# Kernel tuning notes

Measured on AMD Instinct MI355X. Metric: run time of the kernel, lower is better.

Reference implementation:

```python
import jax, jax.numpy as jnp
import numpy as np

_GELU = lambda x: jax.nn.gelu(x, approximate=False)  # torch nn.GELU default = exact erf


def setup_inputs():
    key = jax.random.key(0)
    ks = jax.random.split(key, 32)
    B, H = 16384, 768
    def p(i, shape):
        return jax.random.normal(ks[i], shape, jnp.float32) * 0.02
    return {
        "image_feat": jax.random.normal(ks[0], (B, H), jnp.float32),
        "text_feat": jax.random.normal(ks[1], (B, H), jnp.float32),
        "enhanced_image_feat": jax.random.normal(ks[2], (B, H), jnp.float32),
        "enhanced_text_feat": jax.random.normal(ks[3], (B, H), jnp.float32),
        "missing_type": jax.random.randint(ks[4], (B,), 0, 4),
        # info_encoder: H->256->64
        "info_w1": p(5, (H, 256)), "info_b1": jnp.zeros((256,), jnp.float32),
        "info_w2": p(6, (256, 64)), "info_b2": jnp.zeros((64,), jnp.float32),
        # modality_importance_predictor: H->H/2->1 (dropout inactive at eval)
        "imp_w1": p(7, (H, H // 2)), "imp_b1": jnp.zeros((H // 2,), jnp.float32),
        "imp_w2": p(8, (H // 2, 1)), "imp_b2": jnp.zeros((1,), jnp.float32),
        # feature_discriminator: H->256->64->1
        "disc_w1": p(9, (H, 256)), "disc_b1": jnp.zeros((256,), jnp.float32),
        "disc_w2": p(10, (256, 64)), "disc_b2": jnp.zeros((64,), jnp.float32),
        "disc_w3": p(11, (64, 1)), "disc_b3": jnp.zeros((1,), jnp.float32),
        # consistency_predictor: 2H->H->H/2->1
        "cons_w1": p(12, (2 * H, H)), "cons_b1": jnp.zeros((H,), jnp.float32),
        "cons_w2": p(13, (H, H // 2)), "cons_b2": jnp.zeros((H // 2,), jnp.float32),
        "cons_w3": p(14, (H // 2, 1)), "cons_b3": jnp.zeros((1,), jnp.float32),
        # task_difficulty_predictor: 2H->H->H/2->1
        "diff_w1": p(15, (2 * H, H)), "diff_b1": jnp.zeros((H,), jnp.float32),
        "diff_w2": p(16, (H, H // 2)), "diff_b2": jnp.zeros((H // 2,), jnp.float32),
        "diff_w3": p(17, (H // 2, 1)), "diff_b3": jnp.zeros((1,), jnp.float32),
    }


def _forward(image_feat, text_feat, enhanced_image_feat, enhanced_text_feat,
             info_w1, info_b1, info_w2, info_b2,
             imp_w1, imp_b1, imp_w2, imp_b2,
             disc_w1, disc_b1, disc_w2, disc_b2, disc_w3, disc_b3,
             cons_w1, cons_b1, cons_w2, cons_b2, cons_w3, cons_b3,
             diff_w1, diff_b1, diff_w2, diff_b2, diff_w3, diff_b3):
    sig = jax.nn.sigmoid

    def geometric(f):  # vectorized version of the per-sample python loop
        n = jnp.linalg.norm(f, axis=-1)
        nq = sig((n - 1.0) * 2.0)
        sp = jnp.mean((jnp.abs(f) > 0.01).astype(jnp.float32), axis=-1)
        sq = sig(jnp.std(f, axis=-1, ddof=1) * 10.0 - 1.0)  # torch.std is unbiased
        return (nq + sp + sq) / 3.0

    def information(f):
        enc = _GELU(f @ info_w1 + info_b1) @ info_w2 + info_b2  # [B,64]
        disc = jnp.round(sig(enc) * 10.0).astype(jnp.int32)     # values in 0..10
        # histogram-based entropy == the torch.unique loop (prob = count/64)
        counts = jnp.sum(disc[:, :, None] == jnp.arange(11, dtype=jnp.int32)[None, None, :], axis=1)
        prob = counts.astype(jnp.float32) / enc.shape[-1]
        ent = -jnp.sum(jnp.where(prob > 0, prob * jnp.log(prob + 1e-8), 0.0), axis=-1)
        eq = sig(ent - 2.0)
        # svd of a 1xD matrix has a single singular value = ||f||_2
        n = jnp.linalg.norm(f, axis=-1)
        cq = (n > 0.01).astype(jnp.float32) / f.shape[-1]
        fn = f / jnp.maximum(n, 1e-12)[:, None]  # F.normalize
        dq = sig(jnp.sum(fn * fn, axis=-1) - 0.5)
        return (eq + cq + dq) / 3.0

    def importance(f):
        return sig(_GELU(f @ imp_w1 + imp_b1) @ imp_w2 + imp_b2)[:, 0]

    def discrim(f):
        h = _GELU(f @ disc_w1 + disc_b1)
        h = _GELU(h @ disc_w2 + disc_b2)
        return sig(h @ disc_w3 + disc_b3)[:, 0]

    def head3(f, w1, b1, w2, b2, w3, b3):
        h = _GELU(f @ w1 + b1)
        h = _GELU(h @ w2 + b2)
        return sig(h @ w3 + b3)[:, 0]

    g_img = geometric(image_feat)
    g_txt = geometric(text_feat)
    g_eimg = geometric(enhanced_image_feat)
    g_etxt = geometric(enhanced_text_feat)
    i_img = information(image_feat)
    i_txt = information(text_feat)
    cons_o = head3(jnp.concatenate([image_feat, text_feat], -1), cons_w1, cons_b1, cons_w2, cons_b2, cons_w3, cons_b3)
    cons_e = head3(jnp.concatenate([enhanced_image_feat, enhanced_text_feat], -1), cons_w1, cons_b1, cons_w2, cons_b2, cons_w3, cons_b3)
    imp_i = importance(image_feat)
    imp_t = importance(text_feat)
    imp_ei = importance(enhanced_image_feat)
    imp_et = importance(enhanced_text_feat)
    auth_io = discrim(image_feat)
    auth_ie = discrim(enhanced_image_feat)
    auth_to = discrim(text_feat)
    auth_te = discrim(enhanced_text_feat)
    diff = head3(jnp.concatenate([enhanced_image_feat, enhanced_text_feat], -1), diff_w1, diff_b1, diff_w2, diff_b2, diff_w3, diff_b3)
    overall = (g_img + g_txt + i_img + i_txt + cons_e + (imp_i + imp_t) / 2.0) / 6.0
    return jnp.stack([g_img, g_txt, g_eimg, g_etxt, i_img, i_txt, cons_o, cons_e,
                      imp_i, imp_t, imp_ei, imp_et, auth_io, auth_ie, auth_to, auth_te,
                      diff, overall])  # [18, B]


def reference(image_feat, text_feat, enhanced_image_feat, enhanced_text_feat, missing_type,
              info_w1, info_b1, info_w2, info_b2,
              imp_w1, imp_b1, imp_w2, imp_b2,
              disc_w1, disc_b1, disc_w2, disc_b2, disc_w3, disc_b3,
              cons_w1, cons_b1, cons_w2, cons_b2, cons_w3, cons_b3,
              diff_w1, diff_b1, diff_w2, diff_b2, diff_w3, diff_b3):
    # missing_type is carried by the original forward but never used in the math
    return _forward(image_feat, text_feat, enhanced_image_feat, enhanced_text_feat,
                    info_w1, info_b1, info_w2, info_b2,
                    imp_w1, imp_b1, imp_w2, imp_b2,
                    disc_w1, disc_b1, disc_w2, disc_b2, disc_w3, disc_b3,
                    cons_w1, cons_b1, cons_w2, cons_b2, cons_w3, cons_b3,
                    diff_w1, diff_b1, diff_w2, diff_b2, diff_w3, diff_b3)
```

## Files before the change

kernel.cpp:

```cpp
#include <hip/hip_runtime.h>

typedef unsigned short bfu;
typedef __attribute__((ext_vector_type(8))) __bf16 bf16x8;
typedef __attribute__((ext_vector_type(4))) float f32x4;

__device__ __forceinline__ float bf2f(bfu u) {
    unsigned int x = ((unsigned int)u) << 16;
    return __builtin_bit_cast(float, x);
}
__device__ __forceinline__ bfu f2bf(float f) {
    unsigned int u = __builtin_bit_cast(unsigned int, f);
    unsigned int r = (u + 0x7fffu + ((u >> 16) & 1u)) >> 16;
    return (bfu)r;
}
__device__ __forceinline__ float sigm(float x) { return 1.0f / (1.0f + __expf(-x)); }
__device__ __forceinline__ float gelu_f(float x) {
    const float y = 0.7978845608f * (x + 0.044715f * x * x * x);
    const float t = 1.f - 2.f / (__expf(2.f * y) + 1.f);
    return 0.5f * x * (1.f + t);
}
__device__ __forceinline__ float gelu_x(float x) {
    return 0.5f * x * (1.0f + erff(x * 0.70710678118654752f));
}

__device__ __forceinline__ void async16(const void* g, void* l) {
    __builtin_amdgcn_global_load_lds((const __attribute__((address_space(1))) void*)g,
                                     (__attribute__((address_space(3))) void*)l, 16, 0, 0);
}

struct TDesc { const float* src; bfu* dst; int K, N, blk0; };
struct TPack { TDesc d[9]; };

__global__ __launch_bounds__(256) void transpose_k(TPack p) {
    const int bid = blockIdx.x;
    int j = 0;
#pragma unroll
    for (int i = 1; i < 9; ++i)
        if (bid >= p.d[i].blk0) j = i;
    const TDesc d = p.d[j];
    const int local = bid - d.blk0;
    const int tkn = d.K >> 6;
    const int tk = local % tkn, tn = local / tkn;
    const int k0 = tk * 64, n0 = tn * 64;
    __shared__ float tile[64][65];
    const int tx = threadIdx.x & 63, ty = threadIdx.x >> 6;
#pragma unroll
    for (int i = 0; i < 16; ++i) {
        const int r = ty * 16 + i;
        tile[r][tx] = d.src[(size_t)(k0 + r) * d.N + n0 + tx];
    }
    __syncthreads();
#pragma unroll
    for (int i = 0; i < 16; ++i) {
        const int n = ty * 16 + i;
        d.dst[(size_t)(n0 + n) * d.K + k0 + tx] = f2bf(tile[tx][n]);
    }
}

__global__ __launch_bounds__(256)
void prep_k(float* accz, int nacc, bfu* disc2pad, const float* w3,
            const float* b2, float* w3pad, float* b2pad) {
    const int i = blockIdx.x * 256 + threadIdx.x;
    if (i < nacc) accz[i] = 0.f;
    if (i < 64 * 256) disc2pad[64 * 256 + i] = 0;
    if (i < 128) {
        w3pad[i] = (i < 64) ? w3[i] : 0.f;
        b2pad[i] = (i < 64) ? b2[i] : 0.f;
    }
}

__global__ __launch_bounds__(256)
void geomcast_k(const float* F0, const float* F1, bfu* D0, bfu* D1,
                float* g0, float* g1, float* p0, float* p1) {
    const int z = blockIdx.y;
    const float* F = z ? F1 : F0;
    bfu* D = z ? D1 : D0;
    float* gout = z ? g1 : g0;
    float* part = z ? p1 : p0;
    const int wave = threadIdx.x >> 6, lane = threadIdx.x & 63;
    const int row = blockIdx.x * 4 + wave;
    const float* fr = F + (size_t)row * 768;
    bfu* dr = D + (size_t)row * 768;
    float sum = 0.f, ss = 0.f, cnt = 0.f;
#pragma unroll
    for (int i = 0; i < 3; ++i) {
        const float4 v = *(const float4*)(fr + i * 256 + lane * 4);
        sum += v.x + v.y + v.z + v.w;
        ss += v.x * v.x + v.y * v.y + v.z * v.z + v.w * v.w;
        cnt += ((fabsf(v.x) > 0.01f) ? 1.f : 0.f) + ((fabsf(v.y) > 0.01f) ? 1.f : 0.f) +
               ((fabsf(v.z) > 0.01f) ? 1.f : 0.f) + ((fabsf(v.w) > 0.01f) ? 1.f : 0.f);
        ushort4 b;
        b.x = f2bf(v.x); b.y = f2bf(v.y); b.z = f2bf(v.z); b.w = f2bf(v.w);
        *(ushort4*)(dr + i * 256 + lane * 4) = b;
    }
#pragma unroll
    for (int off = 32; off; off >>= 1) {
        sum += __shfl_xor(sum, off);
        ss  += __shfl_xor(ss, off);
        cnt += __shfl_xor(cnt, off);
    }
    if (lane == 0) {
        const float n = sqrtf(ss);
        const float nq = sigm((n - 1.f) * 2.f);
        const float sp = cnt * (1.f / 768.f);
        float var = (ss - sum * sum * (1.f / 768.f)) * (1.f / 767.f);
        var = fmaxf(var, 0.f);
        const float sq = sigm(sqrtf(var) * 10.f - 1.f);
        gout[row] = (nq + sp + sq) * (1.f / 3.f);
        if (part) {
            const float cq = (n > 0.01f) ? (1.f / 768.f) : 0.f;
            const float nc = fmaxf(n, 1e-12f);
            const float dq = sigm(ss / (nc * nc) - 0.5f);
            part[row] = (cq + dq) * (1.f / 3.f);
        }
    }
}

struct Seg {
    const bfu* A; const bfu* A2;
    const bfu* W;
    const float* bias;
    const float* dotw;
    bfu* C;
    float* acc;
    int ldc, mode, K, Ksplit, lda, Mtiles;
};
struct SegPack { Seg s[13]; };

__global__ __launch_bounds__(256)
void gemm_k(SegPack p) {
    constexpr int BK = 64, MT = 4, NT = 4;
    __shared__ bfu As[128 * BK];
    __shared__ bfu Ws[128 * BK];
    const int NTt = gridDim.x;
    const int g = blockIdx.y * NTt + blockIdx.x;
    const int G8 = NTt * 8;
    const int m = (g / G8) * 8 + (g & 7);
    const int n = (g % G8) >> 3;
    const Seg sg = p.s[n];
    if (m >= sg.Mtiles) return;
    const int t = threadIdx.x;
    const int wave = t >> 6, lane = t & 63;
    const int row_l = lane & 15, kq = lane >> 4;
    const int m0 = m * 128;
    const int wm = wave >> 1, wn = wave & 1;
    const int wrow0 = wm * 64, wcol0 = wn * 64;

    const int r0 = t >> 3;
    const int cc = ((t & 7) ^ (r0 & 7)) << 3;
    const size_t strA = (size_t)32 * sg.lda;
    const size_t strW = (size_t)32 * sg.K;
    const bfu* pA[4];
    const bfu* pW[4];
#pragma unroll
    for (int i = 0; i < 4; ++i) {
        pA[i] = sg.A + (size_t)(m0 + r0) * sg.lda + cc + i * strA;
        pW[i] = sg.W + (size_t)r0 * sg.K + cc + i * strW;
    }
    const int nkt = sg.K >> 6;
    const int ktsw = (sg.Ksplit < sg.K) ? (sg.Ksplit >> 6) : 0x7fffffff;

    f32x4 acc[MT][NT] = {};

    for (int kt = 0; kt < nkt; ++kt) {
        if (kt == ktsw) {
#pragma unroll
            for (int i = 0; i < 4; ++i)
                pA[i] = sg.A2 + (size_t)(m0 + r0) * sg.lda + cc + i * strA;
        }
#pragma unroll
        for (int i = 0; i < 4; ++i)
            async16(pA[i], As + ((i * 256 + wave * 64) << 3));
#pragma unroll
        for (int i = 0; i < 4; ++i)
            async16(pW[i], Ws + ((i * 256 + wave * 64) << 3));
        __syncthreads();
#pragma unroll
        for (int ks = 0; ks < 2; ++ks) {
            bf16x8 af[MT], bfr[NT];
#pragma unroll
            for (int mi = 0; mi < MT; ++mi) {
                const int rA = wrow0 + mi * 16 + row_l;
                af[mi] = *(const bf16x8*)(As + rA * BK + (((ks * 4 + kq) ^ (rA & 7)) << 3));
            }
#pragma unroll
            for (int ni = 0; ni < NT; ++ni) {
                const int rB = wcol0 + ni * 16 + row_l;
                bfr[ni] = *(const bf16x8*)(Ws + rB * BK + (((ks * 4 + kq) ^ (rB & 7)) << 3));
            }
#pragma unroll
            for (int mi = 0; mi < MT; ++mi)
#pragma unroll
                for (int ni = 0; ni < NT; ++ni)
                    acc[mi][ni] = __builtin_amdgcn_mfma_f32_16x16x32_bf16(af[mi], bfr[ni], acc[mi][ni], 0, 0, 0);
        }
        __syncthreads();
#pragma unroll
        for (int i = 0; i < 4; ++i) { pA[i] += BK; pW[i] += BK; }
    }

    if (sg.mode == 0) {
#pragma unroll
        for (int ni = 0; ni < NT; ++ni) {
            const int col = wcol0 + ni * 16 + row_l;
            const float bv = sg.bias[col];
#pragma unroll
            for (int mi = 0; mi < MT; ++mi)
#pragma unroll
                for (int r = 0; r < 4; ++r) {
                    const int row = m0 + wrow0 + mi * 16 + kq * 4 + r;
                    sg.C[(size_t)row * sg.ldc + col] = f2bf(gelu_f(acc[mi][ni][r] + bv));
                }
        }
    } else if (sg.mode == 2) {
#pragma unroll
        for (int ni = 0; ni < NT; ++ni) {
            const int col = wcol0 + ni * 16 + row_l;
            const float bv = sg.bias[col];
#pragma unroll
            for (int mi = 0; mi < MT; ++mi)
#pragma unroll
                for (int r = 0; r < 4; ++r) {
                    const int row = m0 + wrow0 + mi * 16 + kq * 4 + r;
                    sg.C[(size_t)row * sg.ldc + col] = f2bf(gelu_x(acc[mi][ni][r] + bv));
                }
        }
    } else {
#pragma unroll
        for (int mi = 0; mi < MT; ++mi)
#pragma unroll
            for (int r = 0; r < 4; ++r) {
                float s = 0.f;
#pragma unroll
                for (int ni = 0; ni < NT; ++ni) {
                    const int col = wcol0 + ni * 16 + row_l;
                    s += sg.dotw[col] * gelu_f(acc[mi][ni][r] + sg.bias[col]);
                }
                s += __shfl_xor(s, 1); s += __shfl_xor(s, 2);
                s += __shfl_xor(s, 4); s += __shfl_xor(s, 8);
                if (row_l == 0)
                    atomicAdd(sg.acc + m0 + wrow0 + mi * 16 + kq * 4 + r, s);
            }
    }
}

__global__ __launch_bounds__(256)
void gemm64ent_k(const bfu* __restrict__ A, const bfu* __restrict__ W,
                 const float* __restrict__ bias, const float* __restrict__ part,
                 float* out, int B, int K, int lda) {
    constexpr int BK = 64, MT = 2, NT = 4;
    __shared__ __align__(16) float smemf[8320];
    bfu* As = (bfu*)smemf;
    bfu* Ws = (bfu*)smemf + 128 * BK;
    float* ET = smemf;
    const int t = threadIdx.x;
    const int wave = t >> 6, lane = t & 63;
    const int row_l = lane & 15, kq = lane >> 4;
    const int m0 = blockIdx.x * 128;
    const int wrow0 = wave * 32;
    f32x4 acc[MT][NT] = {};
    const int nkt = K / BK;
    for (int kt = 0; kt < nkt; ++kt) {
        const int k0 = kt * BK;
#pragma unroll
        for (int i = 0; i < 4; ++i) {
            const int c = i * 256 + t;
            const int r = c >> 3, s = c & 7;
            const int cc = (s ^ (r & 7)) << 3;
            async16(A + (size_t)(m0 + r) * lda + k0 + cc, As + ((i * 256 + wave * 64) << 3));
        }
#pragma unroll
        for (int i = 0; i < 2; ++i) {
            const int c = i * 256 + t;
            const int r = c >> 3, s = c & 7;
            const int cc = (s ^ (r & 7)) << 3;
            async16(W + (size_t)r * K + k0 + cc, Ws + ((i * 256 + wave * 64) << 3));
        }
        __syncthreads();
#pragma unroll
        for (int ks = 0; ks < 2; ++ks) {
            bf16x8 af[MT], bfr[NT];
#pragma unroll
            for (int mi = 0; mi < MT; ++mi) {
                const int rA = wrow0 + mi * 16 + row_l;
                af[mi] = *(const bf16x8*)(As + rA * BK + (((ks * 4 + kq) ^ (rA & 7)) << 3));
            }
#pragma unroll
            for (int ni = 0; ni < NT; ++ni) {
                const int rB = ni * 16 + row_l;
                bfr[ni] = *(const bf16x8*)(Ws + rB * BK + (((ks * 4 + kq) ^ (rB & 7)) << 3));
            }
#pragma unroll
            for (int mi = 0; mi < MT; ++mi)
#pragma unroll
                for (int ni = 0; ni < NT; ++ni)
                    acc[mi][ni] = __builtin_amdgcn_mfma_f32_16x16x32_bf16(af[mi], bfr[ni], acc[mi][ni], 0, 0, 0);
        }
        __syncthreads();
    }
#pragma unroll
    for (int mi = 0; mi < MT; ++mi)
#pragma unroll
        for (int ni = 0; ni < NT; ++ni) {
            const int col = ni * 16 + row_l;
            const float bv = bias[col];
#pragma unroll
            for (int r = 0; r < 4; ++r)
                ET[(wrow0 + mi * 16 + kq * 4 + r) * 65 + col] = acc[mi][ni][r] + bv;
        }
    __syncthreads();
    if (t < 128) {
        int cnt[11];
#pragma unroll
        for (int b = 0; b < 11; ++b) cnt[b] = 0;
        for (int j = 0; j < 64; ++j) {
            const int d = (int)rintf(sigm(ET[t * 65 + j]) * 10.f);
#pragma unroll
            for (int b = 0; b < 11; ++b) cnt[b] += (d == b);
        }
        float ent = 0.f;
#pragma unroll
        for (int b = 0; b < 11; ++b) {
            if (cnt[b] > 0) {
                const float pp = (float)cnt[b] * (1.f / 64.f);
                ent -= pp * __logf(pp + 1e-8f);
            }
        }
        const int row = m0 + t;
        const int orow = (row < B) ? 4 : 5;
        const int rl = (row < B) ? row : row - B;
        out[(size_t)orow * B + rl] = part[row] + sigm(ent - 2.f) * (1.f / 3.f);
    }
}

__global__ __launch_bounds__(256)
void finalize_k(float* out, const float* a_imp1, const float* a_imp2,
                const float* a_co, const float* a_ce, const float* a_df,
                const float* a_d1, const float* a_d2,
                const float* imp_b2, const float* disc_b3,
                const float* cons_b3, const float* diff_b3, int B) {
    const int i = blockIdx.x * 256 + threadIdx.x;
    if (i >= B) return;
    const float ib = imp_b2[0], db = disc_b3[0], cb = cons_b3[0], fb = diff_b3[0];
    const float o6 = sigm(a_co[i] + cb);
    const float o7 = sigm(a_ce[i] + cb);
    const float o8 = sigm(a_imp1[i] + ib);
    const float o9 = sigm(a_imp1[B + i] + ib);
    out[6 * B + i] = o6;
    out[7 * B + i] = o7;
    out[8 * B + i] = o8;
    out[9 * B + i] = o9;
    out[10 * B + i] = sigm(a_imp2[i] + ib);
    out[11 * B + i] = sigm(a_imp2[B + i] + ib);
    out[12 * B + i] = sigm(a_d1[i] + db);
    out[14 * B + i] = sigm(a_d1[B + i] + db);
    out[13 * B + i] = sigm(a_d2[i] + db);
    out[15 * B + i] = sigm(a_d2[B + i] + db);
    out[16 * B + i] = sigm(a_df[i] + fb);
    const float v = out[0 * B + i] + out[1 * B + i] + out[4 * B + i] + out[5 * B + i] +
                    o7 + 0.5f * (o8 + o9);
    out[17 * B + i] = v * (1.f / 6.f);
}

extern "C" void kernel_launch(void* const* d_in, const int* in_sizes, int n_in,
                              void* d_out, int out_size, void* d_ws, size_t ws_size,
                              hipStream_t stream) {
    const int B = in_sizes[4];
    const int B2 = 2 * B;
    float* out = (float*)d_out;
    const float* img  = (const float*)d_in[0];
    const float* txt  = (const float*)d_in[1];
    const float* eimg = (const float*)d_in[2];
    const float* etxt = (const float*)d_in[3];
    const float* info_w1 = (const float*)d_in[5];  const float* info_b1 = (const float*)d_in[6];
    const float* info_w2 = (const float*)d_in[7];  const float* info_b2 = (const float*)d_in[8];
    const float* imp_w1  = (const float*)d_in[9];  const float* imp_b1  = (const float*)d_in[10];
    const float* imp_w2  = (const float*)d_in[11]; const float* imp_b2  = (const float*)d_in[12];
    const float* disc_w1 = (const float*)d_in[13]; const float* disc_b1 = (const float*)d_in[14];
    const float* disc_w2 = (const float*)d_in[15]; const float* disc_b2 = (const float*)d_in[16];
    const float* disc_w3 = (const float*)d_in[17]; const float* disc_b3 = (const float*)d_in[18];
    const float* cons_w1 = (const float*)d_in[19]; const float* cons_b1 = (const float*)d_in[20];
    const float* cons_w2 = (const float*)d_in[21]; const float* cons_b2 = (const float*)d_in[22];
    const float* cons_w3 = (const float*)d_in[23]; const float* cons_b3 = (const float*)d_in[24];
    const float* diff_w1 = (const float*)d_in[25]; const float* diff_b1 = (const float*)d_in[26];
    const float* diff_w2 = (const float*)d_in[27]; const float* diff_b2 = (const float*)d_in[28];
    const float* diff_w3 = (const float*)d_in[29]; const float* diff_b3 = (const float*)d_in[30];

    char* wsp = (char*)d_ws;
    size_t off = 0;
    auto alloc = [&](size_t bytes) -> void* {
        void* p = wsp + off;
        off += (bytes + 255) & ~(size_t)255;
        return p;
    };
    bfu* info1t = (bfu*)alloc((size_t)256 * 768 * 2);
    bfu* info2t = (bfu*)alloc((size_t)64 * 256 * 2);
    bfu* imp1t  = (bfu*)alloc((size_t)384 * 768 * 2);
    bfu* disc1t = (bfu*)alloc((size_t)256 * 768 * 2);
    bfu* disc2p = (bfu*)alloc((size_t)128 * 256 * 2);
    bfu* cons1t = (bfu*)alloc((size_t)768 * 1536 * 2);
    bfu* cons2t = (bfu*)alloc((size_t)384 * 768 * 2);
    bfu* diff1t = (bfu*)alloc((size_t)768 * 1536 * 2);
    bfu* diff2t = (bfu*)alloc((size_t)384 * 768 * 2);
    float* w3pad = (float*)alloc(128 * 4);
    float* b2pad = (float*)alloc(128 * 4);
    float* part = (float*)alloc((size_t)B2 * 4);
    float* accz = (float*)alloc((size_t)11 * B * 4);
    float* a_imp1 = accz;
    float* a_imp2 = accz + B2;
    float* a_co = accz + 2 * B2;
    float* a_ce = a_co + B;
    float* a_df = a_ce + B;
    float* a_d1 = a_df + B;
    float* a_d2 = a_d1 + B2;
    bfu* fA01 = (bfu*)alloc((size_t)B2 * 768 * 2);
    bfu* X    = (bfu*)alloc((size_t)B * 2048 * 2);
    bfu* Hd   = X;
    bfu* Hi   = X + (size_t)B * 512;
    bfu* Hc_c = X + (size_t)B * 512;
    bfu* Hc_d = X + (size_t)B * 1280;
    (void)ws_size; (void)n_in; (void)out_size;

    prep_k<<<dim3((11 * B + 255) / 256), 256, 0, stream>>>(accz, 11 * B, disc2p,
                                                           disc_w3, disc_b2, w3pad, b2pad);
    TPack tp;
    int blk = 0, ti = 0;
    auto setd = [&](const float* s, bfu* d, int K, int N) {
        tp.d[ti++] = {s, d, K, N, blk};
        blk += (K / 64) * (N / 64);
    };
    setd(info_w1, info1t, 768, 256);
    setd(info_w2, info2t, 256, 64);
    setd(imp_w1, imp1t, 768, 384);
    setd(disc_w1, disc1t, 768, 256);
    setd(disc_w2, disc2p, 256, 64);
    setd(cons_w1, cons1t, 1536, 768);
    setd(cons_w2, cons2t, 768, 384);
    setd(diff_w1, diff1t, 1536, 768);
    setd(diff_w2, diff2t, 768, 384);
    transpose_k<<<dim3(blk), 256, 0, stream>>>(tp);

    auto st_seg = [&](const bfu* A, const bfu* A2, const bfu* W, const float* b,
                      bfu* C, int ldc, int mode, int K, int Ksplit, int lda, int Mt) -> Seg {
        return Seg{A, A2, W, b, nullptr, C, nullptr, ldc, mode, K, Ksplit, lda, Mt};
    };
    auto dt_seg = [&](const bfu* A, const bfu* W, const float* b, const float* dw,
                      float* acc, int K, int lda, int Mt) -> Seg {
        return Seg{A, nullptr, W, b, dw, nullptr, acc, 0, 1, K, K, lda, Mt};
    };
    const bfu* fB = fA01 + (size_t)B * 768;
    const int MT2 = B2 / 128, MT1 = B / 128;

    geomcast_k<<<dim3(B / 4, 2), 256, 0, stream>>>(img, txt, fA01, (bfu*)fB,
                                                   out + 0 * B, out + 1 * B, part, part + B);
    {
        SegPack p;
        p.s[0] = st_seg(fA01, nullptr, info1t, info_b1, Hi, 256, 2, 768, 768, 768, MT2);
        p.s[1] = st_seg(fA01, nullptr, info1t + (size_t)128 * 768, info_b1 + 128, Hi + 128, 256, 2, 768, 768, 768, MT2);
        for (int i = 0; i < 3; ++i)
            p.s[2 + i] = dt_seg(fA01, imp1t + (size_t)128 * i * 768, imp_b1 + 128 * i,
                                imp_w2 + 128 * i, a_imp1, 768, 768, MT2);
        p.s[5] = st_seg(fA01, nullptr, disc1t, disc_b1, Hd, 256, 0, 768, 768, 768, MT2);
        p.s[6] = st_seg(fA01, nullptr, disc1t + (size_t)128 * 768, disc_b1 + 128, Hd + 128, 256, 0, 768, 768, 768, MT2);
        gemm_k<<<dim3(7, MT2), 256, 0, stream>>>(p);
    }
    gemm64ent_k<<<dim3(MT2), 256, 0, stream>>>(Hi, info2t, info_b2, part, out, B, 256, 256);
    {
        SegPack p;
        p.s[0] = dt_seg(Hd, disc2p, b2pad, w3pad, a_d1, 256, 256, MT2);
        for (int i = 0; i < 6; ++i)
            p.s[1 + i] = st_seg(fA01, fB, cons1t + (size_t)128 * i * 1536,
                                cons_b1 + 128 * i, Hc_c + 128 * i, 768, 0, 1536, 768, 768, MT1);
        gemm_k<<<dim3(7, MT2), 256, 0, stream>>>(p);
    }

    geomcast_k<<<dim3(B / 4, 2), 256, 0, stream>>>(eimg, etxt, fA01, (bfu*)fB,
                                                   out + 2 * B, out + 3 * B, nullptr, nullptr);
    {
        SegPack p;
        for (int i = 0; i < 3; ++i)
            p.s[i] = dt_seg(fA01, imp1t + (size_t)128 * i * 768, imp_b1 + 128 * i,
                            imp_w2 + 128 * i, a_imp2, 768, 768, MT2);
        p.s[3] = st_seg(fA01, nullptr, disc1t, disc_b1, Hd, 256, 0, 768, 768, 768, MT2);
        p.s[4] = st_seg(fA01, nullptr, disc1t + (size_t)128 * 768, disc_b1 + 128, Hd + 128, 256, 0, 768, 768, 768, MT2);
        for (int i = 0; i < 3; ++i)
            p.s[5 + i] = dt_seg(Hc_c, cons2t + (size_t)128 * i * 768, cons_b2 + 128 * i,
                                cons_w3 + 128 * i, a_co, 768, 768, MT1);
        gemm_k<<<dim3(8, MT2), 256, 0, stream>>>(p);
    }
    {
        SegPack p;
        p.s[0] = dt_seg(Hd, disc2p, b2pad, w3pad, a_d2, 256, 256, MT2);
        for (int i = 0; i < 6; ++i) {
            p.s[1 + i] = st_seg(fA01, fB, cons1t + (size_t)128 * i * 1536,
                                cons_b1 + 128 * i, Hc_c + 128 * i, 768, 0, 1536, 768, 768, MT1);
            p.s[7 + i] = st_seg(fA01, fB, diff1t + (size_t)128 * i * 1536,
                                diff_b1 + 128 * i, Hc_d + 128 * i, 768, 0, 1536, 768, 768, MT1);
        }
        gemm_k<<<dim3(13, MT2), 256, 0, stream>>>(p);
    }
    {
        SegPack p;
        for (int i = 0; i < 3; ++i) {
            p.s[i]     = dt_seg(Hc_c, cons2t + (size_t)128 * i * 768, cons_b2 + 128 * i,
                                cons_w3 + 128 * i, a_ce, 768, 768, MT1);
            p.s[3 + i] = dt_seg(Hc_d, diff2t + (size_t)128 * i * 768, diff_b2 + 128 * i,
                                diff_w3 + 128 * i, a_df, 768, 768, MT1);
        }
        gemm_k<<<dim3(6, MT1), 256, 0, stream>>>(p);
    }

    finalize_k<<<dim3((B + 255) / 256), 256, 0, stream>>>(out, a_imp1, a_imp2, a_co, a_ce,
                                                          a_df, a_d1, a_d2,
                                                          imp_b2, disc_b3, cons_b3, diff_b3, B);
}
```

Measured before the change: 724.8 us.

## Double-buffer LDS tiles in both GEMM kernels to overlap loads with MFMA

Both the segmented GEMM kernel and the 64-wide entropy GEMM kernel now keep two LDS stage buffers. The next K-tile's async global-to-LDS copy is issued before the MFMA work on the current tile, so memory latency can hide behind compute. The main loop is unrolled by two, and the pointer advance moves into the staging helper. In exchange, LDS use roughly doubles, which may cut occupancy. The loop also assumes an even number of K-tiles.

```diff
diff --git a/kernel.cpp b/kernel.cpp
--- a/kernel.cpp
+++ b/kernel.cpp
@@ -130,8 +130,10 @@
 __global__ __launch_bounds__(256)
 void gemm_k(SegPack p) {
     constexpr int BK = 64, MT = 4, NT = 4;
-    __shared__ bfu As[128 * BK];
-    __shared__ bfu Ws[128 * BK];
+    __shared__ bfu As0[128 * BK];
+    __shared__ bfu Ws0[128 * BK];
+    __shared__ bfu As1[128 * BK];
+    __shared__ bfu Ws1[128 * BK];
     const int NTt = gridDim.x;
     const int g = blockIdx.y * NTt + blockIdx.x;
     const int G8 = NTt * 8;
@@ -162,31 +164,34 @@
 
     f32x4 acc[MT][NT] = {};
 
-    for (int kt = 0; kt < nkt; ++kt) {
-        if (kt == ktsw) {
+    auto stage = [&](bfu* Ad, bfu* Wd, int sn) {
+        if (sn == ktsw) {
 #pragma unroll
             for (int i = 0; i < 4; ++i)
                 pA[i] = sg.A2 + (size_t)(m0 + r0) * sg.lda + cc + i * strA;
         }
 #pragma unroll
         for (int i = 0; i < 4; ++i)
-            async16(pA[i], As + ((i * 256 + wave * 64) << 3));
+            async16(pA[i], Ad + ((i * 256 + wave * 64) << 3));
 #pragma unroll
         for (int i = 0; i < 4; ++i)
-            async16(pW[i], Ws + ((i * 256 + wave * 64) << 3));
-        __syncthreads();
+            async16(pW[i], Wd + ((i * 256 + wave * 64) << 3));
+#pragma unroll
+        for (int i = 0; i < 4; ++i) { pA[i] += BK; pW[i] += BK; }
+    };
+    auto compute = [&](const bfu* Ab, const bfu* Wb) {
 #pragma unroll
         for (int ks = 0; ks < 2; ++ks) {
             bf16x8 af[MT], bfr[NT];
 #pragma unroll
             for (int mi = 0; mi < MT; ++mi) {
                 const int rA = wrow0 + mi * 16 + row_l;
-                af[mi] = *(const bf16x8*)(As + rA * BK + (((ks * 4 + kq) ^ (rA & 7)) << 3));
+                af[mi] = *(const bf16x8*)(Ab + rA * BK + (((ks * 4 + kq) ^ (rA & 7)) << 3));
             }
 #pragma unroll
             for (int ni = 0; ni < NT; ++ni) {
                 const int rB = wcol0 + ni * 16 + row_l;
-                bfr[ni] = *(const bf16x8*)(Ws + rB * BK + (((ks * 4 + kq) ^ (rB & 7)) << 3));
+                bfr[ni] = *(const bf16x8*)(Wb + rB * BK + (((ks * 4 + kq) ^ (rB & 7)) << 3));
             }
 #pragma unroll
             for (int mi = 0; mi < MT; ++mi)
@@ -194,9 +199,17 @@
                 for (int ni = 0; ni < NT; ++ni)
                     acc[mi][ni] = __builtin_amdgcn_mfma_f32_16x16x32_bf16(af[mi], bfr[ni], acc[mi][ni], 0, 0, 0);
         }
+    };
+
+    stage(As0, Ws0, 0);
+    __syncthreads();
+    for (int kt = 0; kt < nkt; kt += 2) {
+        stage(As1, Ws1, kt + 1);
+        compute(As0, Ws0);
         __syncthreads();
-#pragma unroll
-        for (int i = 0; i < 4; ++i) { pA[i] += BK; pW[i] += BK; }
+        if (kt + 2 < nkt) stage(As0, Ws0, kt + 2);
+        compute(As1, Ws1);
+        __syncthreads();
     }
 
     if (sg.mode == 0) {
@@ -249,9 +262,11 @@
                  const float* __restrict__ bias, const float* __restrict__ part,
                  float* out, int B, int K, int lda) {
     constexpr int BK = 64, MT = 2, NT = 4;
-    __shared__ __align__(16) float smemf[8320];
-    bfu* As = (bfu*)smemf;
-    bfu* Ws = (bfu*)smemf + 128 * BK;
+    __shared__ __align__(16) float smemf[12288];
+    bfu* As0 = (bfu*)smemf;
+    bfu* Ws0 = (bfu*)smemf + 128 * BK;
+    bfu* As1 = (bfu*)smemf + 192 * BK;
+    bfu* Ws1 = (bfu*)smemf + 320 * BK;
     float* ET = smemf;
     const int t = threadIdx.x;
     const int wave = t >> 6, lane = t & 63;
@@ -260,35 +275,45 @@
     const int wrow0 = wave * 32;
     f32x4 acc[MT][NT] = {};
     const int nkt = K / BK;
-    for (int kt = 0; kt < nkt; ++kt) {
-        const int k0 = kt * BK;
-#pragma unroll
-        for (int i = 0; i < 4; ++i) {
-            const int c = i * 256 + t;
-            const int r = c >> 3, s = c & 7;
-            const int cc = (s ^ (r & 7)) << 3;
-            async16(A + (size_t)(m0 + r) * lda + k0 + cc, As + ((i * 256 + wave * 64) << 3));
-        }
-#pragma unroll
-        for (int i = 0; i < 2; ++i) {
-            const int c = i * 256 + t;
-            const int r = c >> 3, s = c & 7;
-            const int cc = (s ^ (r & 7)) << 3;
-            async16(W + (size_t)r * K + k0 + cc, Ws + ((i * 256 + wave * 64) << 3));
-        }
-        __syncthreads();
+
+    const int r0 = t >> 3;
+    const int cc = ((t & 7) ^ (r0 & 7)) << 3;
+    const size_t strA = (size_t)32 * lda;
+    const size_t strW = (size_t)32 * K;
+    const bfu* pA[4];
+    const bfu* pW[2];
+#pragma unroll
+    for (int i = 0; i < 4; ++i)
+        pA[i] = A + (size_t)(m0 + r0) * lda + cc + i * strA;
+#pragma unroll
+    for (int i = 0; i < 2; ++i)
+        pW[i] = W + (size_t)r0 * K + cc + i * strW;
+
+    auto stage = [&](bfu* Ad, bfu* Wd) {
+#pragma unroll
+        for (int i = 0; i < 4; ++i)
+            async16(pA[i], Ad + ((i * 256 + wave * 64) << 3));
+#pragma unroll
+        for (int i = 0; i < 2; ++i)
+            async16(pW[i], Wd + ((i * 256 + wave * 64) << 3));
+#pragma unroll
+        for (int i = 0; i < 4; ++i) pA[i] += BK;
+#pragma unroll
+        for (int i = 0; i < 2; ++i) pW[i] += BK;
+    };
+    auto compute = [&](const bfu* Ab, const bfu* Wb) {
 #pragma unroll
         for (int ks = 0; ks < 2; ++ks) {
             bf16x8 af[MT], bfr[NT];
 #pragma unroll
             for (int mi = 0; mi < MT; ++mi) {
                 const int rA = wrow0 + mi * 16 + row_l;
-                af[mi] = *(const bf16x8*)(As + rA * BK + (((ks * 4 + kq) ^ (rA & 7)) << 3));
+                af[mi] = *(const bf16x8*)(Ab + rA * BK + (((ks * 4 + kq) ^ (rA & 7)) << 3));
             }
 #pragma unroll
             for (int ni = 0; ni < NT; ++ni) {
                 const int rB = ni * 16 + row_l;
-                bfr[ni] = *(const bf16x8*)(Ws + rB * BK + (((ks * 4 + kq) ^ (rB & 7)) << 3));
+                bfr[ni] = *(const bf16x8*)(Wb + rB * BK + (((ks * 4 + kq) ^ (rB & 7)) << 3));
             }
 #pragma unroll
             for (int mi = 0; mi < MT; ++mi)
@@ -296,8 +321,19 @@
                 for (int ni = 0; ni < NT; ++ni)
                     acc[mi][ni] = __builtin_amdgcn_mfma_f32_16x16x32_bf16(af[mi], bfr[ni], acc[mi][ni], 0, 0, 0);
         }
+    };
+
+    stage(As0, Ws0);
+    __syncthreads();
+    for (int kt = 0; kt < nkt; kt += 2) {
+        stage(As1, Ws1);
+        compute(As0, Ws0);
         __syncthreads();
-    }
+        if (kt + 2 < nkt) stage(As0, Ws0);
+        compute(As1, Ws1);
+        __syncthreads();
+    }
+
 #pragma unroll
     for (int mi = 0; mi < MT; ++mi)
 #pragma unroll
```

Result: faster. 690.8 us (-4.7%).
